# Kernel tuning notes

Hardware: AMD Instinct MI355X
Metric: run time of the kernel (lower is better)

The kernel has to match this reference:

```python
import jax, jax.numpy as jnp
import numpy as np

N_NODES = 50000
N_EDGES = 800000

def _sage_conv(x, src, dst, W, b, n_nodes):
    # DGL SAGEConv aggregator_type='gcn':
    #   h_neigh = (sum_{u in N(v)} x_u + x_v) / (in_deg(v) + 1)
    #   out = h_neigh @ W.T + b   (fc_self unused for gcn aggregator)
    agg = jax.ops.segment_sum(x[src], dst, num_segments=n_nodes)  # [N, d]
    deg = jax.ops.segment_sum(jnp.ones((src.shape[0],), x.dtype), dst, num_segments=n_nodes)
    h = (agg + x) / (deg + 1.0)[:, None]
    return h @ W.T + b

def setup_inputs() -> dict:
    key = jax.random.key(0)
    ks = jax.random.split(key, 9)
    d_in, d_hid, d_out = 128, 128, 64
    x = jax.random.normal(ks[0], (N_NODES, d_in), dtype=jnp.float32)
    src = jax.random.randint(ks[1], (N_EDGES,), 0, N_NODES, dtype=jnp.int32)
    dst = jax.random.randint(ks[2], (N_EDGES,), 0, N_NODES, dtype=jnp.int32)
    def glorot(k, shape):
        fan = shape[0] + shape[1]
        return jax.random.normal(k, shape, dtype=jnp.float32) * jnp.sqrt(2.0 / fan)
    W1 = glorot(ks[3], (d_hid, d_in))
    b1 = jnp.zeros((d_hid,), jnp.float32)
    W2 = glorot(ks[4], (d_hid, d_hid))
    b2 = jnp.zeros((d_hid,), jnp.float32)
    W3 = glorot(ks[5], (d_out, d_hid))
    b3 = jnp.zeros((d_out,), jnp.float32)
    return {"x": x, "src": src, "dst": dst, "W1": W1, "b1": b1,
            "W2": W2, "b2": b2, "W3": W3, "b3": b3}

def reference(x, src, dst, W1, b1, W2, b2, W3, b3):
    n = x.shape[0]
    h = jax.nn.relu(_sage_conv(x, src, dst, W1, b1, n))
    h = jax.nn.relu(_sage_conv(h, src, dst, W2, b2, n))
    h = jax.nn.sigmoid(_sage_conv(h, src, dst, W3, b3, n))
    return h
```

## Files before the change

kernel.cpp:

```cpp
#include <hip/hip_runtime.h>
#include <hip/hip_bf16.h>
#include <math.h>


#define NFEAT 128
#define BSH   7
#define NBUKP 512
#define EPB2  1024
#define CAP   4000

typedef __attribute__((ext_vector_type(8))) short bf16x8;
typedef __attribute__((ext_vector_type(4))) float f32x4;

__device__ __forceinline__ unsigned short f2bf(float f) {
    unsigned u = __float_as_uint(f);
    u += 0x7fffu + ((u >> 16) & 1u);
    return (unsigned short)(u >> 16);
}
__device__ __forceinline__ float bflo(unsigned u) { return __uint_as_float(u << 16); }
__device__ __forceinline__ float bfhi(unsigned u) { return __uint_as_float(u & 0xffff0000u); }


__global__ __launch_bounds__(256) void build_scatter(const int* __restrict__ src,
                                                     const int* __restrict__ dst,
                                                     int* __restrict__ cursor,
                                                     unsigned long long* __restrict__ pairs,
                                                     int E) {
    __shared__ int hist[NBUKP];
    __shared__ int sc[NBUKP];
    __shared__ int lcur[NBUKP];
    __shared__ int lbase[NBUKP];
    __shared__ unsigned long long stage[EPB2];
    __shared__ int destIdx[EPB2];
    __shared__ int nLocalSh;

    const int t = threadIdx.x;
    hist[t] = 0; hist[t + 256] = 0;
    lcur[t] = 0; lcur[t + 256] = 0;
    __syncthreads();

    const int base = blockIdx.x * EPB2;
    int bb[EPB2 / 256];
    unsigned long long pr[EPB2 / 256];
#pragma unroll
    for (int j = 0; j < EPB2 / 256; ++j) {
        int e = base + t + 256 * j;
        bb[j] = -1;
        if (e < E) {
            int s = src[e], d = dst[e];
            int b = d >> BSH;
            bb[j] = b;
            pr[j] = ((unsigned long long)(unsigned)d << 32) | (unsigned)s;
            atomicAdd(&hist[b], 1);
        }
    }
    __syncthreads();
    sc[t] = hist[t]; sc[t + 256] = hist[t + 256];
    __syncthreads();
    for (int off = 1; off < NBUKP; off <<= 1) {
        int v0 = (t >= off) ? sc[t - off] : 0;
        int v1 = (t + 256 >= off) ? sc[t + 256 - off] : 0;
        __syncthreads();
        sc[t] += v0; sc[t + 256] += v1;
        __syncthreads();
    }
    if (t == 255) nLocalSh = sc[NBUKP - 1];
    sc[t] -= hist[t]; sc[t + 256] -= hist[t + 256];
    for (int b = t; b < NBUKP; b += 256) {
        int h = hist[b];
        if (h > 0) lbase[b] = atomicAdd(&cursor[b], h);
    }
    __syncthreads();
#pragma unroll
    for (int j = 0; j < EPB2 / 256; ++j) {
        int b = bb[j];
        if (b >= 0) {
            int slot = atomicAdd(&lcur[b], 1);
            int spos = sc[b] + slot;
            stage[spos] = pr[j];
            int rel = lbase[b] + slot;
            destIdx[spos] = (rel < CAP) ? (b * CAP + rel) : -1;
        }
    }
    __syncthreads();
    const int nLocal = nLocalSh;
#pragma unroll
    for (int j = 0; j < EPB2 / 256; ++j) {
        int i = t + 256 * j;
        if (i < nLocal && destIdx[i] >= 0) pairs[destIdx[i]] = stage[i];
    }
}


__global__ __launch_bounds__(256) void build_csr(const unsigned long long* __restrict__ pairs,
                                                 const int* __restrict__ cursor,
                                                 int* __restrict__ row_beg,
                                                 int* __restrict__ row_end,
                                                 float* __restrict__ deg_inv,
                                                 int* __restrict__ col_idx, int N) {
    __shared__ unsigned long long pairsL[CAP];
    __shared__ int srcS[CAP];
    __shared__ int nhist[128];
    __shared__ int npref[128];
    __shared__ int ncur[128];

    const int t = threadIdx.x;
    const int b = blockIdx.x;
    const int nodeBase = b << BSH;
    const int eBeg = b * CAP;
    int eCnt = cursor[b];
    if (eCnt > CAP) eCnt = CAP;

    if (t < 128) { nhist[t] = 0; ncur[t] = 0; }
    __syncthreads();

    for (int i = t; i < eCnt; i += 256) {
        unsigned long long p = pairs[eBeg + i];
        pairsL[i] = p;
        atomicAdd(&nhist[(int)(p >> 32) - nodeBase], 1);
    }
    __syncthreads();
    if (t < 128) npref[t] = nhist[t];
    __syncthreads();
    for (int off = 1; off < 128; off <<= 1) {
        int v = (t < 128 && t >= off) ? npref[t - off] : 0;
        __syncthreads();
        if (t < 128) npref[t] += v;
        __syncthreads();
    }
    if (t < 128) npref[t] -= nhist[t];
    if (t < 128 && nodeBase + t < N) {
        row_beg[nodeBase + t] = eBeg + npref[t];
        row_end[nodeBase + t] = eBeg + npref[t] + nhist[t];
        deg_inv[nodeBase + t] = 1.0f / (float)(nhist[t] + 1);
    }
    __syncthreads();
    for (int i = t; i < eCnt; i += 256) {
        unsigned long long p = pairsL[i];
        int d = (int)(p >> 32) - nodeBase;
        int slot = atomicAdd(&ncur[d], 1);
        srcS[npref[d] + slot] = (int)(unsigned)p;
    }
    __syncthreads();
    for (int i = t; i < eCnt; i += 256) col_idx[eBeg + i] = srcS[i];
}


__global__ __launch_bounds__(256) void cvt_all_kernel(const float* __restrict__ x,
                                                      const float* __restrict__ W1,
                                                      const float* __restrict__ W2,
                                                      const float* __restrict__ W3,
                                                      ushort* __restrict__ xb,
                                                      ushort* __restrict__ w1,
                                                      ushort* __restrict__ w2,
                                                      ushort* __restrict__ w3,
                                                      int* __restrict__ cursor, int nbuk,
                                                      int nx, int n1, int n2, int n3) {
    int i = blockIdx.x * blockDim.x + threadIdx.x;
    if (i < nbuk) cursor[i] = 0;
    const float* src; ushort* dst; int off;
    if (i < nx)                      { src = x;  dst = xb; off = i; }
    else if (i < nx + n1)            { src = W1; dst = w1; off = i - nx; }
    else if (i < nx + n1 + n2)       { src = W2; dst = w2; off = i - nx - n1; }
    else if (i < nx + n1 + n2 + n3)  { src = W3; dst = w3; off = i - nx - n1 - n2; }
    else return;
    float4 f = *(const float4*)(src + (size_t)off * 4);
    *(ushort4*)(dst + (size_t)off * 4) = make_ushort4(f2bf(f.x), f2bf(f.y), f2bf(f.z), f2bf(f.w));
}


#define ACC8(u)                                                     \
    a0 += bflo((u).x); a1 += bfhi((u).x);                           \
    a2 += bflo((u).y); a3 += bfhi((u).y);                           \
    a4 += bflo((u).z); a5 += bfhi((u).z);                           \
    a6 += bflo((u).w); a7 += bfhi((u).w);

template<int SECOND>
__global__ __launch_bounds__(256) void fused_agg_gemm_kernel(
        const ushort* __restrict__ Xb,
        const int* __restrict__ row_beg,
        const int* __restrict__ row_end,
        const float* __restrict__ deg_inv,
        const ushort* __restrict__ Wb,
        const float* __restrict__ bias,
        const ushort* __restrict__ W3b,
        const int* __restrict__ col_idx,
        ushort* __restrict__ outB, int N) {
    __shared__ ushort A[16][136];
    __shared__ ushort H2[SECOND ? 16 : 1][136];

    const int t    = threadIdx.x;
    const int w    = t >> 6;
    const int lane = t & 63;
    const int g    = lane >> 4;
    const int f    = lane & 15;
    const int base = blockIdx.x * 16;
    const uint4* X4 = (const uint4*)Xb;

#pragma unroll
    for (int i = 0; i < 4; ++i) {
        const int v = base + w * 4 + i;
        if (v < N) {
            const int beg = row_beg[v];
            const int end = row_end[v];

            float a0 = 0.f, a1 = 0.f, a2 = 0.f, a3 = 0.f;
            float a4 = 0.f, a5 = 0.f, a6 = 0.f, a7 = 0.f;
            int e = beg + g;
            for (; e + 12 < end; e += 16) {
                int s0 = col_idx[e];
                int s1 = col_idx[e + 4];
                int s2 = col_idx[e + 8];
                int s3 = col_idx[e + 12];
                uint4 u0 = X4[(size_t)s0 * 16 + f];
                uint4 u1 = X4[(size_t)s1 * 16 + f];
                uint4 u2 = X4[(size_t)s2 * 16 + f];
                uint4 u3 = X4[(size_t)s3 * 16 + f];
                ACC8(u0); ACC8(u1); ACC8(u2); ACC8(u3);
            }
            for (; e < end; e += 4) {
                uint4 u = X4[(size_t)col_idx[e] * 16 + f];
                ACC8(u);
            }
            a0 += __shfl_xor(a0, 16, 64); a0 += __shfl_xor(a0, 32, 64);
            a1 += __shfl_xor(a1, 16, 64); a1 += __shfl_xor(a1, 32, 64);
            a2 += __shfl_xor(a2, 16, 64); a2 += __shfl_xor(a2, 32, 64);
            a3 += __shfl_xor(a3, 16, 64); a3 += __shfl_xor(a3, 32, 64);
            a4 += __shfl_xor(a4, 16, 64); a4 += __shfl_xor(a4, 32, 64);
            a5 += __shfl_xor(a5, 16, 64); a5 += __shfl_xor(a5, 32, 64);
            a6 += __shfl_xor(a6, 16, 64); a6 += __shfl_xor(a6, 32, 64);
            a7 += __shfl_xor(a7, 16, 64); a7 += __shfl_xor(a7, 32, 64);
            if (g == 0) {
                uint4 us = X4[(size_t)v * 16 + f];
                float inv = deg_inv[v];
                uint4 r;
                r.x = (unsigned)f2bf((a0 + bflo(us.x)) * inv) | ((unsigned)f2bf((a1 + bfhi(us.x)) * inv) << 16);
                r.y = (unsigned)f2bf((a2 + bflo(us.y)) * inv) | ((unsigned)f2bf((a3 + bfhi(us.y)) * inv) << 16);
                r.z = (unsigned)f2bf((a4 + bflo(us.z)) * inv) | ((unsigned)f2bf((a5 + bfhi(us.z)) * inv) << 16);
                r.w = (unsigned)f2bf((a6 + bflo(us.w)) * inv) | ((unsigned)f2bf((a7 + bfhi(us.w)) * inv) << 16);
                ((uint4*)&A[w * 4 + i][0])[f] = r;
            }
        }
    }
    __syncthreads();

    const int m    = lane & 15;
    const int quad = lane >> 4;
    f32x4 acc0 = {0.f, 0.f, 0.f, 0.f};
    f32x4 acc1 = {0.f, 0.f, 0.f, 0.f};
    {
        const ushort* arow = &A[m][quad * 8];
        const ushort* wrow = Wb + (size_t)(w * 32 + m) * NFEAT + quad * 8;
#pragma unroll
        for (int k0 = 0; k0 < NFEAT; k0 += 32) {
            bf16x8 a  = *(const bf16x8*)(arow + k0);
            bf16x8 bA = *(const bf16x8*)(wrow + k0);
            bf16x8 bB = *(const bf16x8*)(wrow + 16 * NFEAT + k0);
            acc0 = __builtin_amdgcn_mfma_f32_16x16x32_bf16(a, bA, acc0, 0, 0, 0);
            acc1 = __builtin_amdgcn_mfma_f32_16x16x32_bf16(a, bB, acc1, 0, 0, 0);
        }
    }
    const float bv0 = bias[w * 32 + m];
    const float bv1 = bias[w * 32 + 16 + m];

    if (!SECOND) {
#pragma unroll
        for (int r = 0; r < 4; ++r) {
            int row = base + quad * 4 + r;
            if (row < N) {
                outB[(size_t)row * NFEAT + w * 32 + m]      = f2bf(fmaxf(acc0[r] + bv0, 0.f));
                outB[(size_t)row * NFEAT + w * 32 + 16 + m] = f2bf(fmaxf(acc1[r] + bv1, 0.f));
            }
        }
    } else {
#pragma unroll
        for (int r = 0; r < 4; ++r) {
            H2[quad * 4 + r][w * 32 + m]      = f2bf(fmaxf(acc0[r] + bv0, 0.f));
            H2[quad * 4 + r][w * 32 + 16 + m] = f2bf(fmaxf(acc1[r] + bv1, 0.f));
        }
        __syncthreads();
        f32x4 acc3 = {0.f, 0.f, 0.f, 0.f};
        const ushort* hrow  = &H2[m][quad * 8];
        const ushort* w3row = W3b + (size_t)(w * 16 + m) * NFEAT + quad * 8;
#pragma unroll
        for (int k0 = 0; k0 < NFEAT; k0 += 32) {
            bf16x8 a = *(const bf16x8*)(hrow + k0);
            bf16x8 b = *(const bf16x8*)(w3row + k0);
            acc3 = __builtin_amdgcn_mfma_f32_16x16x32_bf16(a, b, acc3, 0, 0, 0);
        }
#pragma unroll
        for (int r = 0; r < 4; ++r) {
            int row = base + quad * 4 + r;
            if (row < N) outB[(size_t)row * 64 + w * 16 + m] = f2bf(acc3[r]);
        }
    }
}


__global__ __launch_bounds__(256) void agg64_sigmoid_kernel(const ushort* __restrict__ Gb,
                                                            const int* __restrict__ row_beg,
                                                            const int* __restrict__ row_end,
                                                            const float* __restrict__ deg_inv,
                                                            const int* __restrict__ col_idx,
                                                            const float* __restrict__ bias,
                                                            float* __restrict__ out, int N) {
    const int wp   = blockIdx.x * (blockDim.x >> 6) + (threadIdx.x >> 6);
    const int lane = threadIdx.x & 63;
    const int half = lane >> 5;
    const int hl   = lane & 31;
    const int v    = wp * 2 + half;
    const bool act = (v < N);

    int beg = 0, end = 0;
    if (act) { beg = row_beg[v]; end = row_end[v]; }
    const int deg = end - beg;
    const unsigned* Gu = (const unsigned*)Gb;

    int cidx = 0;
    if (hl < deg) cidx = col_idx[beg + hl];

    float a0 = 0.f, a1 = 0.f, b0 = 0.f, b1 = 0.f;
    float c0 = 0.f, c1 = 0.f, d0 = 0.f, d1 = 0.f;
    const int nfast = deg < 32 ? deg : 32;
    int j = 0;
    for (; j + 3 < nfast; j += 4) {
        int s0 = __shfl(cidx, j + 0, 32);
        int s1 = __shfl(cidx, j + 1, 32);
        int s2 = __shfl(cidx, j + 2, 32);
        int s3 = __shfl(cidx, j + 3, 32);
        unsigned u0 = Gu[(size_t)s0 * 32 + hl];
        unsigned u1 = Gu[(size_t)s1 * 32 + hl];
        unsigned u2 = Gu[(size_t)s2 * 32 + hl];
        unsigned u3 = Gu[(size_t)s3 * 32 + hl];
        a0 += bflo(u0); a1 += bfhi(u0);
        b0 += bflo(u1); b1 += bfhi(u1);
        c0 += bflo(u2); c1 += bfhi(u2);
        d0 += bflo(u3); d1 += bfhi(u3);
    }
    for (; j < nfast; ++j) {
        int s0 = __shfl(cidx, j, 32);
        unsigned u0 = Gu[(size_t)s0 * 32 + hl];
        a0 += bflo(u0); a1 += bfhi(u0);
    }
    for (int e = beg + 32; e < end; ++e) {
        unsigned u0 = Gu[(size_t)col_idx[e] * 32 + hl];
        a0 += bflo(u0); a1 += bfhi(u0);
    }
    if (act) {
        unsigned us = Gu[(size_t)v * 32 + hl];
        float inv = deg_inv[v];
        float r0 = (a0 + b0 + c0 + d0 + bflo(us)) * inv + bias[hl * 2 + 0];
        float r1 = (a1 + b1 + c1 + d1 + bfhi(us)) * inv + bias[hl * 2 + 1];
        r0 = 1.0f / (1.0f + __expf(-r0));
        r1 = 1.0f / (1.0f + __expf(-r1));
        *(float2*)(out + (size_t)v * 64 + hl * 2) = make_float2(r0, r1);
    }
}


static inline size_t align256(size_t x) { return (x + 255) & ~(size_t)255; }

extern "C" void kernel_launch(void* const* d_in, const int* in_sizes, int n_in,
                              void* d_out, int out_size, void* d_ws, size_t ws_size,
                              hipStream_t stream) {
    const float* x   = (const float*)d_in[0];
    const int*   src = (const int*)d_in[1];
    const int*   dst = (const int*)d_in[2];
    const float* W1  = (const float*)d_in[3];
    const float* b1  = (const float*)d_in[4];
    const float* W2  = (const float*)d_in[5];
    const float* b2  = (const float*)d_in[6];
    const float* W3  = (const float*)d_in[7];
    const float* b3  = (const float*)d_in[8];
    float*       out = (float*)d_out;

    const int N = in_sizes[0] / NFEAT;
    const int E = in_sizes[1];
    const int D_OUT = in_sizes[7] / NFEAT;
    const int NBUK = (N + (1 << BSH) - 1) >> BSH;
    const int SBLK = (E + EPB2 - 1) / EPB2;

    char* ws = (char*)d_ws;
    int* row_beg      = (int*)ws;  ws += align256((size_t)N * 4);
    int* row_end      = (int*)ws;  ws += align256((size_t)N * 4);
    float* deg_inv    = (float*)ws; ws += align256((size_t)N * 4);
    int* cursor       = (int*)ws;  ws += align256((size_t)NBUK * 4);
    int* col_idx      = (int*)ws;  ws += align256((size_t)NBUK * CAP * 4);
    ushort* w1bf      = (ushort*)ws; ws += align256((size_t)NFEAT * NFEAT * 2);
    ushort* w2bf      = (ushort*)ws; ws += align256((size_t)NFEAT * NFEAT * 2);
    ushort* w3bf      = (ushort*)ws; ws += align256((size_t)D_OUT * NFEAT * 2);
    ushort* xbf       = (ushort*)ws; ws += align256((size_t)N * NFEAT * 2);
    ushort* h1bf      = (ushort*)ws; ws += align256((size_t)N * NFEAT * 2);
    ushort* gbf = xbf;
    unsigned long long* pairs = (unsigned long long*)h1bf;

    const int nx = N * NFEAT / 4;
    const int n1 = NFEAT * NFEAT / 4, n2 = NFEAT * NFEAT / 4, n3 = D_OUT * NFEAT / 4;
    cvt_all_kernel<<<(nx + n1 + n2 + n3 + 255) / 256, 256, 0, stream>>>(
        x, W1, W2, W3, xbf, w1bf, w2bf, w3bf, cursor, NBUK, nx, n1, n2, n3);

    build_scatter<<<SBLK, 256, 0, stream>>>(src, dst, cursor, pairs, E);
    build_csr<<<NBUK, 256, 0, stream>>>(pairs, cursor, row_beg, row_end, deg_inv, col_idx, N);

    const int fusedBlocks = (N + 15) / 16;
    const int agg64Blocks = (N + 7) / 8;

    fused_agg_gemm_kernel<0><<<fusedBlocks, 256, 0, stream>>>(
        xbf, row_beg, row_end, deg_inv, w1bf, b1, nullptr, col_idx, h1bf, N);
    fused_agg_gemm_kernel<1><<<fusedBlocks, 256, 0, stream>>>(
        h1bf, row_beg, row_end, deg_inv, w2bf, b2, w3bf, col_idx, gbf, N);
    agg64_sigmoid_kernel<<<agg64Blocks, 256, 0, stream>>>(
        gbf, row_beg, row_end, deg_inv, col_idx, b3, out, N);
}
```

Before: 233.6 us.

## Assign one node per 16-lane group in aggregation and unroll gathers by eight

The fused aggregate+GEMM kernel's gather changes from splitting each node's edges across four 16-lane groups (then shuffle-reducing) to giving each 16-lane group its own node. Column indices are preloaded into registers and broadcast by shuffles, with eight row loads in flight per iteration. The final layer's gather loop also gets an 8-way unrolled path. The aim is to drop the cross-group reductions, cut dependent index loads and raise memory-level parallelism, at the cost of more registers and load imbalance between groups whose nodes have very different degrees.

```diff
diff --git a/kernel.cpp b/kernel.cpp
--- a/kernel.cpp
+++ b/kernel.cpp
@@ -197,49 +197,63 @@
     const int base = blockIdx.x * 16;
     const uint4* X4 = (const uint4*)Xb;
 
-#pragma unroll
-    for (int i = 0; i < 4; ++i) {
-        const int v = base + w * 4 + i;
+    {
+        const int v = base + w * 4 + g;
+        const int beg = (v < N) ? row_beg[v] : 0;
+        const int end = (v < N) ? row_end[v] : 0;
+        const int deg = end - beg;
+
+        uint4 us = (v < N) ? X4[(size_t)v * 16 + f] : make_uint4(0, 0, 0, 0);
+        float inv = (v < N) ? deg_inv[v] : 0.f;
+
+        int c0 = 0, c1 = 0;
+        if (f < deg)      c0 = col_idx[beg + f];
+        if (f + 16 < deg) c1 = col_idx[beg + 16 + f];
+
+        float a0 = 0.f, a1 = 0.f, a2 = 0.f, a3 = 0.f;
+        float a4 = 0.f, a5 = 0.f, a6 = 0.f, a7 = 0.f;
+
+        const int nf = deg < 32 ? deg : 32;
+        int j = 0;
+        for (; j + 7 < nf; j += 8) {
+            const int cc = (j & 16) ? c1 : c0;
+            int s0 = __shfl(cc, (j & 15) + 0, 16);
+            int s1 = __shfl(cc, (j & 15) + 1, 16);
+            int s2 = __shfl(cc, (j & 15) + 2, 16);
+            int s3 = __shfl(cc, (j & 15) + 3, 16);
+            int s4 = __shfl(cc, (j & 15) + 4, 16);
+            int s5 = __shfl(cc, (j & 15) + 5, 16);
+            int s6 = __shfl(cc, (j & 15) + 6, 16);
+            int s7 = __shfl(cc, (j & 15) + 7, 16);
+            uint4 u0 = X4[(size_t)s0 * 16 + f];
+            uint4 u1 = X4[(size_t)s1 * 16 + f];
+            uint4 u2 = X4[(size_t)s2 * 16 + f];
+            uint4 u3 = X4[(size_t)s3 * 16 + f];
+            uint4 u4 = X4[(size_t)s4 * 16 + f];
+            uint4 u5 = X4[(size_t)s5 * 16 + f];
+            uint4 u6 = X4[(size_t)s6 * 16 + f];
+            uint4 u7 = X4[(size_t)s7 * 16 + f];
+            ACC8(u0); ACC8(u1); ACC8(u2); ACC8(u3);
+            ACC8(u4); ACC8(u5); ACC8(u6); ACC8(u7);
+        }
+        for (; j < nf; ++j) {
+            const int cc = (j & 16) ? c1 : c0;
+            int s0 = __shfl(cc, j & 15, 16);
+            uint4 u = X4[(size_t)s0 * 16 + f];
+            ACC8(u);
+        }
+        for (int e = beg + 32; e < end; ++e) {
+            uint4 u = X4[(size_t)col_idx[e] * 16 + f];
+            ACC8(u);
+        }
+
         if (v < N) {
-            const int beg = row_beg[v];
-            const int end = row_end[v];
-
-            float a0 = 0.f, a1 = 0.f, a2 = 0.f, a3 = 0.f;
-            float a4 = 0.f, a5 = 0.f, a6 = 0.f, a7 = 0.f;
-            int e = beg + g;
-            for (; e + 12 < end; e += 16) {
-                int s0 = col_idx[e];
-                int s1 = col_idx[e + 4];
-                int s2 = col_idx[e + 8];
-                int s3 = col_idx[e + 12];
-                uint4 u0 = X4[(size_t)s0 * 16 + f];
-                uint4 u1 = X4[(size_t)s1 * 16 + f];
-                uint4 u2 = X4[(size_t)s2 * 16 + f];
-                uint4 u3 = X4[(size_t)s3 * 16 + f];
-                ACC8(u0); ACC8(u1); ACC8(u2); ACC8(u3);
-            }
-            for (; e < end; e += 4) {
-                uint4 u = X4[(size_t)col_idx[e] * 16 + f];
-                ACC8(u);
-            }
-            a0 += __shfl_xor(a0, 16, 64); a0 += __shfl_xor(a0, 32, 64);
-            a1 += __shfl_xor(a1, 16, 64); a1 += __shfl_xor(a1, 32, 64);
-            a2 += __shfl_xor(a2, 16, 64); a2 += __shfl_xor(a2, 32, 64);
-            a3 += __shfl_xor(a3, 16, 64); a3 += __shfl_xor(a3, 32, 64);
-            a4 += __shfl_xor(a4, 16, 64); a4 += __shfl_xor(a4, 32, 64);
-            a5 += __shfl_xor(a5, 16, 64); a5 += __shfl_xor(a5, 32, 64);
-            a6 += __shfl_xor(a6, 16, 64); a6 += __shfl_xor(a6, 32, 64);
-            a7 += __shfl_xor(a7, 16, 64); a7 += __shfl_xor(a7, 32, 64);
-            if (g == 0) {
-                uint4 us = X4[(size_t)v * 16 + f];
-                float inv = deg_inv[v];
-                uint4 r;
-                r.x = (unsigned)f2bf((a0 + bflo(us.x)) * inv) | ((unsigned)f2bf((a1 + bfhi(us.x)) * inv) << 16);
-                r.y = (unsigned)f2bf((a2 + bflo(us.y)) * inv) | ((unsigned)f2bf((a3 + bfhi(us.y)) * inv) << 16);
-                r.z = (unsigned)f2bf((a4 + bflo(us.z)) * inv) | ((unsigned)f2bf((a5 + bfhi(us.z)) * inv) << 16);
-                r.w = (unsigned)f2bf((a6 + bflo(us.w)) * inv) | ((unsigned)f2bf((a7 + bfhi(us.w)) * inv) << 16);
-                ((uint4*)&A[w * 4 + i][0])[f] = r;
-            }
+            uint4 r;
+            r.x = (unsigned)f2bf((a0 + bflo(us.x)) * inv) | ((unsigned)f2bf((a1 + bfhi(us.x)) * inv) << 16);
+            r.y = (unsigned)f2bf((a2 + bflo(us.y)) * inv) | ((unsigned)f2bf((a3 + bfhi(us.y)) * inv) << 16);
+            r.z = (unsigned)f2bf((a4 + bflo(us.z)) * inv) | ((unsigned)f2bf((a5 + bfhi(us.z)) * inv) << 16);
+            r.w = (unsigned)f2bf((a6 + bflo(us.w)) * inv) | ((unsigned)f2bf((a7 + bfhi(us.w)) * inv) << 16);
+            ((uint4*)&A[w * 4 + g][0])[f] = r;
         }
     }
     __syncthreads();
@@ -323,6 +337,32 @@
     float c0 = 0.f, c1 = 0.f, d0 = 0.f, d1 = 0.f;
     const int nfast = deg < 32 ? deg : 32;
     int j = 0;
+    for (; j + 7 < nfast; j += 8) {
+        int s0 = __shfl(cidx, j + 0, 32);
+        int s1 = __shfl(cidx, j + 1, 32);
+        int s2 = __shfl(cidx, j + 2, 32);
+        int s3 = __shfl(cidx, j + 3, 32);
+        int s4 = __shfl(cidx, j + 4, 32);
+        int s5 = __shfl(cidx, j + 5, 32);
+        int s6 = __shfl(cidx, j + 6, 32);
+        int s7 = __shfl(cidx, j + 7, 32);
+        unsigned u0 = Gu[(size_t)s0 * 32 + hl];
+        unsigned u1 = Gu[(size_t)s1 * 32 + hl];
+        unsigned u2 = Gu[(size_t)s2 * 32 + hl];
+        unsigned u3 = Gu[(size_t)s3 * 32 + hl];
+        unsigned u4 = Gu[(size_t)s4 * 32 + hl];
+        unsigned u5 = Gu[(size_t)s5 * 32 + hl];
+        unsigned u6 = Gu[(size_t)s6 * 32 + hl];
+        unsigned u7 = Gu[(size_t)s7 * 32 + hl];
+        a0 += bflo(u0); a1 += bfhi(u0);
+        b0 += bflo(u1); b1 += bfhi(u1);
+        c0 += bflo(u2); c1 += bfhi(u2);
+        d0 += bflo(u3); d1 += bfhi(u3);
+        a0 += bflo(u4); a1 += bfhi(u4);
+        b0 += bflo(u5); b1 += bfhi(u5);
+        c0 += bflo(u6); c1 += bfhi(u6);
+        d0 += bflo(u7); d1 += bfhi(u7);
+    }
     for (; j + 3 < nfast; j += 4) {
         int s0 = __shfl(cidx, j + 0, 32);
         int s1 = __shfl(cidx, j + 1, 32);
```

New measurement: 227.5 us. 2.6% less time.
